# Optimization experiments

Hardware: AMD Instinct MI355X
Metric: run time of the kernel (lower is better)

The kernel has to match this reference:

```python
import jax, jax.numpy as jnp
import numpy as np

B, T, C = 8, 2048, 1024
NEG = -1.0e10  # torch fill value -10000000000.0

def setup_inputs() -> dict:
    key = jax.random.key(0)
    k1, k2, k3 = jax.random.split(key, 3)
    return {
        "query": jax.random.normal(k1, (B, T, C), dtype=jnp.float32),
        "keys": jax.random.normal(k2, (B, T, C), dtype=jnp.float32),
        "values": jax.random.normal(k3, (B, T, C), dtype=jnp.float32),
        "mask": jnp.ones((B, T), dtype=jnp.float32),
        "m": 128,
    }

def reference(query, keys, values, mask, m):
    num_tags = query.shape[-1]
    scale = 1.0 / np.sqrt(num_tags).astype(np.float32)
    # energy[b,t,s] = <query[b,t], keys[b,s]>
    energy = jnp.einsum('btc,bsc->bts', query, keys)
    if m > 0:
        idx = jnp.arange(query.shape[1])
        band = jnp.where(jnp.abs(idx[:, None] - idx[None, :]) <= m,
                         jnp.float32(0.0), jnp.float32(NEG))
        energy = energy + band[None, :, :]
    # torch applies scale AFTER adding mask (mul_ after the add), then softmax
    att = jax.nn.softmax(energy * scale, axis=2)
    lc = jnp.einsum('bts,bsc->btc', att, values)
    lc = lc * mask[:, :, None]
    # form == 'max': max over channel dim, then sum over time -> [B]
    return lc.max(axis=2).sum(axis=1)
```

## Files before the change

kernel.cpp:

```cpp
#include <hip/hip_runtime.h>
#include <math.h>

#define T_DIM 2048
#define C_DIM 1024
#define B_DIM 8
#define TB    32
#define KROW  72
#define PROW  296

typedef float f32x4 __attribute__((ext_vector_type(4)));
typedef short s16x8 __attribute__((ext_vector_type(8)));

__device__ __forceinline__ unsigned short f2bf(float x) {
    union { float f; unsigned u; } v; v.f = x;
    unsigned r = v.u + 0x7fffu + ((v.u >> 16) & 1u);
    return (unsigned short)(r >> 16);
}
__device__ __forceinline__ unsigned pk2(float a, float b) {
    return (unsigned)f2bf(a) | ((unsigned)f2bf(b) << 16);
}

__device__ __forceinline__ void gll16(const unsigned short* g, short* l) {
    __builtin_amdgcn_global_load_lds(
        (const __attribute__((address_space(1))) unsigned int*)g,
        (__attribute__((address_space(3))) unsigned int*)l,
        16, 0, 0);
}

__global__ __launch_bounds__(256)
void tile_qk(const float* __restrict__ Q, const float* __restrict__ K,
             unsigned short* __restrict__ Qt, unsigned short* __restrict__ Kt)
{
    const int bx   = blockIdx.x;
    const int tile = bx & 127;
    const float* src = (bx < 128) ? Q : K;
    unsigned short* dst = (bx < 128) ? Qt : Kt;
    const int b    = blockIdx.y;
    const int tid  = threadIdx.x;
    const int w = tid >> 6, l = tid & 63, g = l >> 4, ln = l & 15;
    const float* src_row = src + (size_t)(b * T_DIM + tile * 16 + ln) * C_DIM;
#pragma unroll
    for (int kki = 0; kki < 8; ++kki) {
        const int kk = kki * 4 + w;
        const float4* p = (const float4*)(src_row + kk * 32 + g * 8);
        float4 x = p[0], y = p[1];
        uint4 o;
        o.x = pk2(x.x, x.y); o.y = pk2(x.z, x.w);
        o.z = pk2(y.x, y.y); o.w = pk2(y.z, y.w);
        *(uint4*)(dst + (size_t)(((b * 128 + tile) * 32 + kk) * 64 + l) * 8) = o;
    }
}

__global__ __launch_bounds__(256)
void transpose_vx(const float* __restrict__ V, unsigned short* __restrict__ out,
                  int frag_mode)
{
    __shared__ float buf[64 * 67];
    const int t0 = blockIdx.x * 64;
    const int c0 = blockIdx.y * 64;
    const int b  = blockIdx.z;
    const float* Vb = V + (size_t)b * T_DIM * C_DIM;

    for (int i = threadIdx.x; i < 64 * 64; i += 256) {
        const int r = i >> 6, c = i & 63;
        buf[r * 67 + c] = Vb[(size_t)(t0 + r) * C_DIM + c0 + c];
    }
    __syncthreads();
    const int t8 = threadIdx.x & 7;
    const int cl = threadIdx.x >> 3;
#pragma unroll
    for (int half = 0; half < 2; ++half) {
        const int c_loc = cl + half * 32;
        float v[8];
#pragma unroll
        for (int j = 0; j < 8; ++j) v[j] = buf[(t8 * 8 + j) * 67 + c_loc];
        uint4 o;
        o.x = pk2(v[0], v[1]); o.y = pk2(v[2], v[3]);
        o.z = pk2(v[4], v[5]); o.w = pk2(v[6], v[7]);
        if (frag_mode) {
            const int ct = (c0 + c_loc) >> 4, lnv = c_loc & 15;
            const int g = t8 & 3, sg = (t0 >> 5) + (t8 >> 2);
            *(uint4*)(out + (size_t)(((b * 64 + ct) * 64 + sg) * 64 + g * 16 + lnv) * 8) = o;
        } else {
            *(uint4*)(out + (size_t)(b * C_DIM + c0 + c_loc) * T_DIM + t0 + t8 * 8) = o;
        }
    }
}

__global__ __launch_bounds__(256, 2)
void attn_band_tiled(const unsigned short* __restrict__ Qt,
                     const unsigned short* __restrict__ Kt,
                     const unsigned short* __restrict__ Vtt,
                     const float* __restrict__ Mask, const int* __restrict__ m_ptr,
                     float* __restrict__ wsrow)
{
    __shared__ __align__(16) short SMEM[30208];
    __shared__ float pmax[64], psum[64], red[64];
    short* Kbuf = SMEM;
    short* P    = SMEM;
    short* Vbuf = SMEM + 9728;

    const int h = blockIdx.x;
    const int logical = (h & 7) * 64 + (h >> 3);
    const int b  = logical >> 6;
    const int t0 = (logical & 63) * TB;

    const int tid = threadIdx.x;
    const int w = tid >> 6, lane = tid & 63, g = lane >> 4, ln = lane & 15;
    const int th = w >> 1, sh = w & 1;
    const int m  = m_ptr[0];

    const int s_lo = max(0, t0 - m);
    const int s_hi = min(T_DIM - 1, t0 + TB - 1 + m);
    const int sg0  = s_lo >> 5;
    const int tq0  = t0 >> 4;

    const unsigned short* Qtb = Qt  + (size_t)b * 128 * 32 * 512;
    const unsigned short* Ktb = Kt  + (size_t)b * 128 * 32 * 512;
    const unsigned short* Vtb = Vtt + (size_t)b * 64 * 64 * 512;

    f32x4 E[9];
    f32x4 zed = {0.f, 0.f, 0.f, 0.f};
#pragma unroll
    for (int i = 0; i < 9; ++i) E[i] = zed;

#define STAGE1(KN, NB)                                                              \
    {                                                                               \
        short* dstb = Kbuf + (NB) * 10240;                                          \
        _Pragma("unroll")                                                           \
        for (int f5 = 0; f5 < 5; ++f5) {                                            \
            const int f = w * 5 + f5;                                               \
            const unsigned short* gp;                                               \
            if (f < 18) gp = Ktb + ((size_t)(min(sg0 * 2 + f, 127) * 32 + (KN)) * 64 + lane) * 8; \
            else        gp = Qtb + ((size_t)((tq0 + (f - 18)) * 32 + (KN)) * 64 + lane) * 8;      \
            gll16(gp, dstb + f * 512);                                              \
        }                                                                           \
    }

    STAGE1(0, 0);
    __syncthreads();

#pragma unroll 2
    for (int kk = 0; kk < 32; ++kk) {
        const int cur = kk & 1;
        if (kk < 31) STAGE1(kk + 1, cur ^ 1);
        const short* cb = Kbuf + cur * 10240;
        s16x8 aq = *(const s16x8*)(cb + (18 + th) * 512 + lane * 8);
#pragma unroll
        for (int i = 0; i < 9; ++i) {
            s16x8 bk = *(const s16x8*)(cb + (sh * 9 + i) * 512 + lane * 8);
            E[i] = __builtin_amdgcn_mfma_f32_16x16x32_bf16(aq, bk, E[i], 0, 0, 0);
        }
        __syncthreads();
    }

    const float scale = 0.03125f;
    const int rowb = th * 16 + g * 4;
    float lm[4];
#pragma unroll
    for (int r = 0; r < 4; ++r) lm[r] = -INFINITY;
    const int s_base = s_lo + sh * 144 + ln;
#pragma unroll
    for (int i = 0; i < 9; ++i) {
        const int s = s_base + i * 16;
#pragma unroll
        for (int r = 0; r < 4; ++r) {
            const int t = t0 + rowb + r;
            int d = t - s; d = d < 0 ? -d : d;
            const bool valid = (s <= s_hi) && (d <= m);
            float e = valid ? E[i][r] : -INFINITY;
            E[i][r] = e;
            lm[r] = fmaxf(lm[r], e);
        }
    }
#pragma unroll
    for (int r = 0; r < 4; ++r)
#pragma unroll
        for (int dd = 1; dd < 16; dd <<= 1) lm[r] = fmaxf(lm[r], __shfl_xor(lm[r], dd));
    if (ln == 0) {
#pragma unroll
        for (int r = 0; r < 4; ++r) pmax[sh * 32 + rowb + r] = lm[r];
    }
    __syncthreads();
    float Mr[4], sum[4];
#pragma unroll
    for (int r = 0; r < 4; ++r) {
        Mr[r] = fmaxf(pmax[rowb + r], pmax[32 + rowb + r]) * scale;
        sum[r] = 0.f;
    }
#pragma unroll
    for (int i = 0; i < 9; ++i)
#pragma unroll
        for (int r = 0; r < 4; ++r) {
            float e = __expf(E[i][r] * scale - Mr[r]);
            E[i][r] = e;
            sum[r] += e;
        }
#pragma unroll
    for (int r = 0; r < 4; ++r)
#pragma unroll
        for (int dd = 1; dd < 16; dd <<= 1) sum[r] += __shfl_xor(sum[r], dd);
    if (ln == 0) {
#pragma unroll
        for (int r = 0; r < 4; ++r) psum[sh * 32 + rowb + r] = sum[r];
    }
    __syncthreads();
    float inv[4];
#pragma unroll
    for (int r = 0; r < 4; ++r) inv[r] = 1.0f / (psum[rowb + r] + psum[32 + rowb + r]);
#pragma unroll
    for (int i = 0; i < 9; ++i) {
        const int col = sh * 144 + i * 16 + ln;
#pragma unroll
        for (int r = 0; r < 4; ++r)
            P[(rowb + r) * PROW + col] = (short)f2bf(E[i][r] * inv[r]);
    }
    __syncthreads();

    s16x8 pa[9];
#pragma unroll
    for (int kg = 0; kg < 9; ++kg)
        pa[kg] = *(const s16x8*)(P + (th * 16 + ln) * PROW + kg * 32 + g * 8);

    int sgc[9];
#pragma unroll
    for (int kg = 0; kg < 9; ++kg) sgc[kg] = min(sg0 + kg, 63);

    float maskv[4], rmax[4];
#pragma unroll
    for (int r = 0; r < 4; ++r) {
        maskv[r] = Mask[(size_t)b * T_DIM + t0 + rowb + r];
        rmax[r]  = -INFINITY;
    }

#define STAGE3(S, NB)                                                               \
    {                                                                               \
        const int q_ = (S) >> 1;                                                    \
        short* dstb = Vbuf + (NB) * 10240;                                          \
        const int ct_ = q_ * 4 + w;                                                 \
        if (((S) & 1) == 0) {                                                       \
            _Pragma("unroll")                                                       \
            for (int e = 0; e < 5; ++e)                                             \
                gll16(Vtb + ((size_t)(ct_ * 64 + sgc[e]) * 64 + lane) * 8,          \
                      dstb + (w * 5 + e) * 512);                                    \
        } else {                                                                    \
            _Pragma("unroll")                                                       \
            for (int e = 0; e < 4; ++e)                                             \
                gll16(Vtb + ((size_t)(ct_ * 64 + sgc[5 + e]) * 64 + lane) * 8,      \
                      dstb + (w * 4 + e) * 512);                                    \
        }                                                                           \
    }

    STAGE3(0, 0);
    __syncthreads();

    f32x4 O0 = zed, O1 = zed;
#pragma unroll 2
    for (int s = 0; s < 32; ++s) {
        const int cur = s & 1;
        if (s < 31) STAGE3(s + 1, cur ^ 1);
        const short* vb = Vbuf + cur * 10240;
        if ((s & 1) == 0) {
            O0 = zed; O1 = zed;
#pragma unroll
            for (int e = 0; e < 5; ++e) {
                s16x8 bv0 = *(const s16x8*)(vb + ((sh * 2    ) * 5 + e) * 512 + lane * 8);
                s16x8 bv1 = *(const s16x8*)(vb + ((sh * 2 + 1) * 5 + e) * 512 + lane * 8);
                O0 = __builtin_amdgcn_mfma_f32_16x16x32_bf16(pa[e], bv0, O0, 0, 0, 0);
                O1 = __builtin_amdgcn_mfma_f32_16x16x32_bf16(pa[e], bv1, O1, 0, 0, 0);
            }
        } else {
#pragma unroll
            for (int e = 0; e < 4; ++e) {
                s16x8 bv0 = *(const s16x8*)(vb + ((sh * 2    ) * 4 + e) * 512 + lane * 8);
                s16x8 bv1 = *(const s16x8*)(vb + ((sh * 2 + 1) * 4 + e) * 512 + lane * 8);
                O0 = __builtin_amdgcn_mfma_f32_16x16x32_bf16(pa[5 + e], bv0, O0, 0, 0, 0);
                O1 = __builtin_amdgcn_mfma_f32_16x16x32_bf16(pa[5 + e], bv1, O1, 0, 0, 0);
            }
#pragma unroll
            for (int r = 0; r < 4; ++r) {
                rmax[r] = fmaxf(rmax[r], O0[r] * maskv[r]);
                rmax[r] = fmaxf(rmax[r], O1[r] * maskv[r]);
            }
        }
        __syncthreads();
    }

#pragma unroll
    for (int r = 0; r < 4; ++r)
#pragma unroll
        for (int dd = 1; dd < 16; dd <<= 1) rmax[r] = fmaxf(rmax[r], __shfl_xor(rmax[r], dd));
    if (ln == 0) {
#pragma unroll
        for (int r = 0; r < 4; ++r) red[sh * 32 + rowb + r] = rmax[r];
    }
    __syncthreads();
    if (tid < 32)
        wsrow[(size_t)b * T_DIM + t0 + tid] = fmaxf(red[tid], red[32 + tid]);
}

__global__ __launch_bounds__(256, 2)
void attn_band_mfma(const float* __restrict__ Q, const float* __restrict__ K,
                    const unsigned short* __restrict__ Vt,
                    const float* __restrict__ Mask, const int* __restrict__ m_ptr,
                    float* __restrict__ wsrow)
{
    __shared__ __align__(16) char smem_raw[57600];
    short* SM = (short*)smem_raw;
    short* Kc = SM;
    short* Qc = SM + 288 * KROW;
    short* P  = SM;
    short* Vl = SM + 32 * PROW;
    float* pmax = (float*)(smem_raw + 56832);
    float* psum = pmax + 64;
    float* red  = psum + 64;

    const int h = blockIdx.x;
    const int logical = (h & 7) * 64 + (h >> 3);
    const int b  = logical >> 6;
    const int t0 = (logical & 63) * TB;

    const int tid = threadIdx.x;
    const int w = tid >> 6, lane = tid & 63, g = lane >> 4, ln = lane & 15;
    const int th = w >> 1, sh = w & 1;
    const int m  = m_ptr[0];

    const int s_lo = max(0, t0 - m);
    const int s_hi = min(T_DIM - 1, t0 + TB - 1 + m);

    const float* Qb = Q + (size_t)b * T_DIM * C_DIM;
    const float* Kb = K + (size_t)b * T_DIM * C_DIM;
    const unsigned short* Vtb = Vt + (size_t)b * C_DIM * T_DIM;

    f32x4 E[9];
    f32x4 zed = {0.f, 0.f, 0.f, 0.f};
#pragma unroll
    for (int i = 0; i < 9; ++i) E[i] = zed;

    for (int cc = 0; cc < C_DIM / 64; ++cc) {
        const int c0 = cc * 64;
        __syncthreads();
        for (int u = tid; u < 288 * 8; u += 256) {
            const int su = u >> 3, un = u & 7;
            const int s = min(s_lo + su, T_DIM - 1);
            const float4* src = (const float4*)(Kb + (size_t)s * C_DIM + c0 + un * 8);
            float4 x = src[0], y = src[1];
            uint4 o; o.x = pk2(x.x, x.y); o.y = pk2(x.z, x.w);
            o.z = pk2(y.x, y.y); o.w = pk2(y.z, y.w);
            *(uint4*)(Kc + su * KROW + un * 8) = o;
        }
        {
            const int su = tid >> 3, un = tid & 7;
            const float4* src = (const float4*)(Qb + (size_t)(t0 + su) * C_DIM + c0 + un * 8);
            float4 x = src[0], y = src[1];
            uint4 o; o.x = pk2(x.x, x.y); o.y = pk2(x.z, x.w);
            o.z = pk2(y.x, y.y); o.w = pk2(y.z, y.w);
            *(uint4*)(Qc + su * KROW + un * 8) = o;
        }
        __syncthreads();
        s16x8 aq[2];
#pragma unroll
        for (int kk = 0; kk < 2; ++kk)
            aq[kk] = *(const s16x8*)(Qc + (th * 16 + ln) * KROW + kk * 32 + g * 8);
#pragma unroll
        for (int i = 0; i < 9; ++i) {
            const int srow2 = (sh * 9 + i) * 16 + ln;
#pragma unroll
            for (int kk = 0; kk < 2; ++kk) {
                s16x8 bk = *(const s16x8*)(Kc + srow2 * KROW + kk * 32 + g * 8);
                E[i] = __builtin_amdgcn_mfma_f32_16x16x32_bf16(aq[kk], bk, E[i], 0, 0, 0);
            }
        }
    }

    const float scale = 0.03125f;
    const int rowb = th * 16 + g * 4;
    float lm[4];
#pragma unroll
    for (int r = 0; r < 4; ++r) lm[r] = -INFINITY;
    const int s_base = s_lo + sh * 144 + ln;
#pragma unroll
    for (int i = 0; i < 9; ++i) {
        const int s = s_base + i * 16;
#pragma unroll
        for (int r = 0; r < 4; ++r) {
            const int t = t0 + rowb + r;
            int d = t - s; d = d < 0 ? -d : d;
            const bool valid = (s <= s_hi) && (d <= m);
            float e = valid ? E[i][r] : -INFINITY;
            E[i][r] = e;
            lm[r] = fmaxf(lm[r], e);
        }
    }
#pragma unroll
    for (int r = 0; r < 4; ++r)
#pragma unroll
        for (int dd = 1; dd < 16; dd <<= 1) lm[r] = fmaxf(lm[r], __shfl_xor(lm[r], dd));
    if (ln == 0) {
#pragma unroll
        for (int r = 0; r < 4; ++r) pmax[sh * 32 + rowb + r] = lm[r];
    }
    __syncthreads();
    float Mr[4], sum[4];
#pragma unroll
    for (int r = 0; r < 4; ++r) {
        Mr[r] = fmaxf(pmax[rowb + r], pmax[32 + rowb + r]) * scale;
        sum[r] = 0.f;
    }
#pragma unroll
    for (int i = 0; i < 9; ++i)
#pragma unroll
        for (int r = 0; r < 4; ++r) {
            float e = __expf(E[i][r] * scale - Mr[r]);
            E[i][r] = e;
            sum[r] += e;
        }
#pragma unroll
    for (int r = 0; r < 4; ++r)
#pragma unroll
        for (int dd = 1; dd < 16; dd <<= 1) sum[r] += __shfl_xor(sum[r], dd);
    if (ln == 0) {
#pragma unroll
        for (int r = 0; r < 4; ++r) psum[sh * 32 + rowb + r] = sum[r];
    }
    __syncthreads();
    float inv[4];
#pragma unroll
    for (int r = 0; r < 4; ++r) inv[r] = 1.0f / (psum[rowb + r] + psum[32 + rowb + r]);
#pragma unroll
    for (int i = 0; i < 9; ++i) {
        const int col = sh * 144 + i * 16 + ln;
#pragma unroll
        for (int r = 0; r < 4; ++r)
            P[(rowb + r) * PROW + col] = (short)f2bf(E[i][r] * inv[r]);
    }
    __syncthreads();

    s16x8 pa[9];
#pragma unroll
    for (int kg = 0; kg < 9; ++kg)
        pa[kg] = *(const s16x8*)(P + (th * 16 + ln) * PROW + kg * 32 + g * 8);

    float maskv[4], rmax[4];
#pragma unroll
    for (int r = 0; r < 4; ++r) {
        maskv[r] = Mask[(size_t)b * T_DIM + t0 + rowb + r];
        rmax[r]  = -INFINITY;
    }

    for (int cc = 0; cc < C_DIM / 64; ++cc) {
        __syncthreads();
        for (int i2 = tid; i2 < 64 * 36; i2 += 256) {
            const int cr = i2 / 36, un = i2 - cr * 36;
            const int sb = min(s_lo + un * 8, T_DIM - 8);
            uint4 x = *(const uint4*)(Vtb + (size_t)(cc * 64 + cr) * T_DIM + sb);
            *(uint4*)(Vl + cr * PROW + un * 8) = x;
        }
        __syncthreads();
#pragma unroll
        for (int nbi = 0; nbi < 2; ++nbi) {
            const int crow = sh * 32 + nbi * 16 + ln;
            f32x4 O = zed;
#pragma unroll
            for (int kg = 0; kg < 9; ++kg) {
                s16x8 bv = *(const s16x8*)(Vl + crow * PROW + kg * 32 + g * 8);
                O = __builtin_amdgcn_mfma_f32_16x16x32_bf16(pa[kg], bv, O, 0, 0, 0);
            }
#pragma unroll
            for (int r = 0; r < 4; ++r)
                rmax[r] = fmaxf(rmax[r], O[r] * maskv[r]);
        }
    }
#pragma unroll
    for (int r = 0; r < 4; ++r)
#pragma unroll
        for (int dd = 1; dd < 16; dd <<= 1) rmax[r] = fmaxf(rmax[r], __shfl_xor(rmax[r], dd));
    if (ln == 0) {
#pragma unroll
        for (int r = 0; r < 4; ++r) red[sh * 32 + rowb + r] = rmax[r];
    }
    __syncthreads();
    if (tid < 32)
        wsrow[(size_t)b * T_DIM + t0 + tid] = fmaxf(red[tid], red[32 + tid]);
}

__global__ void reduce_b(const float* __restrict__ ws, float* __restrict__ out)
{
    const int b = blockIdx.x;
    float s = 0.f;
    for (int t = threadIdx.x; t < T_DIM; t += 256) s += ws[(size_t)b * T_DIM + t];
#pragma unroll
    for (int dd = 32; dd > 0; dd >>= 1) s += __shfl_xor(s, dd);
    __shared__ float acc[4];
    if ((threadIdx.x & 63) == 0) acc[threadIdx.x >> 6] = s;
    __syncthreads();
    if (threadIdx.x == 0) out[b] = acc[0] + acc[1] + acc[2] + acc[3];
}

extern "C" void kernel_launch(void* const* d_in, const int* in_sizes, int n_in,
                              void* d_out, int out_size, void* d_ws, size_t ws_size,
                              hipStream_t stream)
{
    const float* Q    = (const float*)d_in[0];
    const float* K    = (const float*)d_in[1];
    const float* V    = (const float*)d_in[2];
    const float* Mask = (const float*)d_in[3];
    const int*   m    = (const int*)d_in[4];
    float* out = (float*)d_out;

    const size_t frag_bytes = (size_t)B_DIM * T_DIM * C_DIM * 2;
    const size_t need_main  = 3 * frag_bytes + (size_t)B_DIM * T_DIM * 4;

    if (ws_size >= need_main) {
        unsigned short* Qt  = (unsigned short*)d_ws;
        unsigned short* Kt  = (unsigned short*)((char*)d_ws + frag_bytes);
        unsigned short* Vtt = (unsigned short*)((char*)d_ws + 2 * frag_bytes);
        float* wsrow = (float*)((char*)d_ws + 3 * frag_bytes);
        tile_qk<<<dim3(256, B_DIM), 256, 0, stream>>>(Q, K, Qt, Kt);
        transpose_vx<<<dim3(T_DIM / 64, C_DIM / 64, B_DIM), 256, 0, stream>>>(V, Vtt, 1);
        attn_band_tiled<<<dim3((T_DIM / TB) * B_DIM), 256, 0, stream>>>(Qt, Kt, Vtt, Mask, m, wsrow);
        reduce_b<<<B_DIM, 256, 0, stream>>>(wsrow, out);
    } else {
        unsigned short* Vt = (unsigned short*)d_ws;
        float* wsrow = (float*)((char*)d_ws + frag_bytes);
        transpose_vx<<<dim3(T_DIM / 64, C_DIM / 64, B_DIM), 256, 0, stream>>>(V, Vt, 0);
        attn_band_mfma<<<dim3((T_DIM / TB) * B_DIM), 256, 0, stream>>>(Q, K, Vt, Mask, m, wsrow);
        reduce_b<<<B_DIM, 256, 0, stream>>>(wsrow, out);
    }
}
```

Baseline: 114.9 us.

## Read fp32 Q directly in attention kernel and convert K row-major

Removes the separate Q bf16 fragment conversion pass. The attention kernel now loads fp32 Q straight into LDS with global_load_lds and packs it to bf16 in registers. K is converted to bf16 in plain row-major order by a simpler elementwise kernel, and the attention kernel gathers K fragments with strided row loads instead of pre-tiled fragments. This saves one full-tensor read/write round-trip and a workspace buffer. In exchange it adds per-iteration conversion work, higher Q load bandwidth in the hot loop, and less coalesced K fragment loads.

```diff
diff --git a/kernel.cpp b/kernel.cpp
--- a/kernel.cpp
+++ b/kernel.cpp
@@ -20,7 +20,7 @@
     return (unsigned)f2bf(a) | ((unsigned)f2bf(b) << 16);
 }
 
-__device__ __forceinline__ void gll16(const unsigned short* g, short* l) {
+__device__ __forceinline__ void gll16(const void* g, void* l) {
     __builtin_amdgcn_global_load_lds(
         (const __attribute__((address_space(1))) unsigned int*)g,
         (__attribute__((address_space(3))) unsigned int*)l,
@@ -28,27 +28,16 @@
 }
 
 __global__ __launch_bounds__(256)
-void tile_qk(const float* __restrict__ Q, const float* __restrict__ K,
-             unsigned short* __restrict__ Qt, unsigned short* __restrict__ Kt)
+void conv_k(const float* __restrict__ K, unsigned short* __restrict__ Kb)
 {
-    const int bx   = blockIdx.x;
-    const int tile = bx & 127;
-    const float* src = (bx < 128) ? Q : K;
-    unsigned short* dst = (bx < 128) ? Qt : Kt;
-    const int b    = blockIdx.y;
-    const int tid  = threadIdx.x;
-    const int w = tid >> 6, l = tid & 63, g = l >> 4, ln = l & 15;
-    const float* src_row = src + (size_t)(b * T_DIM + tile * 16 + ln) * C_DIM;
-#pragma unroll
-    for (int kki = 0; kki < 8; ++kki) {
-        const int kk = kki * 4 + w;
-        const float4* p = (const float4*)(src_row + kk * 32 + g * 8);
-        float4 x = p[0], y = p[1];
-        uint4 o;
-        o.x = pk2(x.x, x.y); o.y = pk2(x.z, x.w);
-        o.z = pk2(y.x, y.y); o.w = pk2(y.z, y.w);
-        *(uint4*)(dst + (size_t)(((b * 128 + tile) * 32 + kk) * 64 + l) * 8) = o;
-    }
+    const size_t base = (size_t)blockIdx.y * T_DIM * C_DIM
+                      + (size_t)blockIdx.x * 2048 + (size_t)threadIdx.x * 8;
+    const float4* src = (const float4*)(K + base);
+    float4 x = src[0], y = src[1];
+    uint4 o;
+    o.x = pk2(x.x, x.y); o.y = pk2(x.z, x.w);
+    o.z = pk2(y.x, y.y); o.w = pk2(y.z, y.w);
+    *(uint4*)(Kb + base) = o;
 }
 
 __global__ __launch_bounds__(256)
@@ -88,17 +77,15 @@
 }
 
 __global__ __launch_bounds__(256, 2)
-void attn_band_tiled(const unsigned short* __restrict__ Qt,
-                     const unsigned short* __restrict__ Kt,
+void attn_band_tiled(const float* __restrict__ Q,
+                     const unsigned short* __restrict__ Kb,
                      const unsigned short* __restrict__ Vtt,
                      const float* __restrict__ Mask, const int* __restrict__ m_ptr,
                      float* __restrict__ wsrow)
 {
-    __shared__ __align__(16) short SMEM[30208];
+    __shared__ __align__(16) char RAW[60416];
     __shared__ float pmax[64], psum[64], red[64];
-    short* Kbuf = SMEM;
-    short* P    = SMEM;
-    short* Vbuf = SMEM + 9728;
+    short* P = (short*)RAW;
 
     const int h = blockIdx.x;
     const int logical = (h & 7) * 64 + (h >> 3);
@@ -113,10 +100,9 @@
     const int s_lo = max(0, t0 - m);
     const int s_hi = min(T_DIM - 1, t0 + TB - 1 + m);
     const int sg0  = s_lo >> 5;
-    const int tq0  = t0 >> 4;
-
-    const unsigned short* Qtb = Qt  + (size_t)b * 128 * 32 * 512;
-    const unsigned short* Ktb = Kt  + (size_t)b * 128 * 32 * 512;
+
+    const float*          Qg  = Q   + (size_t)b * T_DIM * C_DIM;
+    const unsigned short* Kg  = Kb  + (size_t)b * T_DIM * C_DIM;
     const unsigned short* Vtb = Vtt + (size_t)b * 64 * 64 * 512;
 
     f32x4 E[9];
@@ -124,17 +110,23 @@
 #pragma unroll
     for (int i = 0; i < 9; ++i) E[i] = zed;
 
-#define STAGE1(KN, NB)                                                              \
-    {                                                                               \
-        short* dstb = Kbuf + (NB) * 10240;                                          \
-        _Pragma("unroll")                                                           \
-        for (int f5 = 0; f5 < 5; ++f5) {                                            \
-            const int f = w * 5 + f5;                                               \
-            const unsigned short* gp;                                               \
-            if (f < 18) gp = Ktb + ((size_t)(min(sg0 * 2 + f, 127) * 32 + (KN)) * 64 + lane) * 8; \
-            else        gp = Qtb + ((size_t)((tq0 + (f - 18)) * 32 + (KN)) * 64 + lane) * 8;      \
-            gll16(gp, dstb + f * 512);                                              \
-        }                                                                           \
+#define STAGE1(KN, NB)                                                               \
+    {                                                                                \
+        short* kd = (short*)(RAW) + (NB) * 9216;                                     \
+        _Pragma("unroll")                                                            \
+        for (int f5 = 0; f5 < 5; ++f5) {                                             \
+            const int f = w * 5 + f5;                                                \
+            if (f < 18) {                                                            \
+                const int row = min(sg0 * 2 + f, 127) * 16 + ln;                     \
+                gll16(Kg + (size_t)row * C_DIM + (KN) * 32 + g * 8, kd + f * 512);   \
+            }                                                                        \
+        }                                                                            \
+        {                                                                            \
+            const int tt = w >> 1, hh = w & 1;                                       \
+            const float* qs = Qg + (size_t)(t0 + tt * 16 + ln) * C_DIM               \
+                                 + (KN) * 32 + g * 8 + hh * 4;                       \
+            gll16(qs, (float*)(RAW + 36864) + (NB) * 1024 + (tt * 2 + hh) * 256);    \
+        }                                                                            \
     }
 
     STAGE1(0, 0);
@@ -144,8 +136,14 @@
     for (int kk = 0; kk < 32; ++kk) {
         const int cur = kk & 1;
         if (kk < 31) STAGE1(kk + 1, cur ^ 1);
-        const short* cb = Kbuf + cur * 10240;
-        s16x8 aq = *(const s16x8*)(cb + (18 + th) * 512 + lane * 8);
+        const short* cb = (const short*)(RAW) + cur * 9216;
+        const float* qb = (const float*)(RAW + 36864) + cur * 1024;
+        f32x4 qlo = *(const f32x4*)(qb + (th * 2    ) * 256 + lane * 4);
+        f32x4 qhi = *(const f32x4*)(qb + (th * 2 + 1) * 256 + lane * 4);
+        uint4 aqi;
+        aqi.x = pk2(qlo[0], qlo[1]); aqi.y = pk2(qlo[2], qlo[3]);
+        aqi.z = pk2(qhi[0], qhi[1]); aqi.w = pk2(qhi[2], qhi[3]);
+        s16x8 aq = *(s16x8*)&aqi;
 #pragma unroll
         for (int i = 0; i < 9; ++i) {
             s16x8 bk = *(const s16x8*)(cb + (sh * 9 + i) * 512 + lane * 8);
@@ -217,6 +215,7 @@
     }
     __syncthreads();
 
+    short* Vbuf = (short*)(RAW + 19456);
     s16x8 pa[9];
 #pragma unroll
     for (int kg = 0; kg < 9; ++kg)
@@ -509,16 +508,15 @@
     float* out = (float*)d_out;
 
     const size_t frag_bytes = (size_t)B_DIM * T_DIM * C_DIM * 2;
-    const size_t need_main  = 3 * frag_bytes + (size_t)B_DIM * T_DIM * 4;
+    const size_t need_main  = 2 * frag_bytes + (size_t)B_DIM * T_DIM * 4;
 
     if (ws_size >= need_main) {
-        unsigned short* Qt  = (unsigned short*)d_ws;
-        unsigned short* Kt  = (unsigned short*)((char*)d_ws + frag_bytes);
-        unsigned short* Vtt = (unsigned short*)((char*)d_ws + 2 * frag_bytes);
-        float* wsrow = (float*)((char*)d_ws + 3 * frag_bytes);
-        tile_qk<<<dim3(256, B_DIM), 256, 0, stream>>>(Q, K, Qt, Kt);
+        unsigned short* Kb  = (unsigned short*)d_ws;
+        unsigned short* Vtt = (unsigned short*)((char*)d_ws + frag_bytes);
+        float* wsrow = (float*)((char*)d_ws + 2 * frag_bytes);
+        conv_k<<<dim3(1024, B_DIM), 256, 0, stream>>>(K, Kb);
         transpose_vx<<<dim3(T_DIM / 64, C_DIM / 64, B_DIM), 256, 0, stream>>>(V, Vtt, 1);
-        attn_band_tiled<<<dim3((T_DIM / TB) * B_DIM), 256, 0, stream>>>(Qt, Kt, Vtt, Mask, m, wsrow);
+        attn_band_tiled<<<dim3((T_DIM / TB) * B_DIM), 256, 0, stream>>>(Q, Kb, Vtt, Mask, m, wsrow);
         reduce_b<<<B_DIM, 256, 0, stream>>>(wsrow, out);
     } else {
         unsigned short* Vt = (unsigned short*)d_ws;
```

Measured after the change: 104.3 us. 9.2% less time.
